# Performance work log

Hardware: AMD Instinct MI355X
Metric: run time of the kernel (lower is better)

## Reference

```python
import jax, jax.numpy as jnp
import numpy as np

B, CIN, H, W = 32, 16, 32, 128
COUT = 128


def _run_direction(x_hwbc, p):
    # x_hwbc: (H, W, B, CIN); scan order is raster (top-to-bottom, left-to-right).
    # Predecessors: dim0 = cell above (previous row), dim1 = cell to the left.
    xi = jnp.einsum('hwbc,oc->hwbo', x_hwbc, p['w_ii'])
    xf = jnp.einsum('hwbc,oc->hwbo', x_hwbc, p['w_if'])
    xg = jnp.einsum('hwbc,oc->hwbo', x_hwbc, p['w_ig'])
    xo = jnp.einsum('hwbc,oc->hwbo', x_hwbc, p['w_io'])
    Wdim, Bdim = x_hwbc.shape[1], x_hwbc.shape[2]
    O = p['w_hi'].shape[0]
    ws0, ws1 = p['ws'][0], p['ws'][1]

    def branch(xi_, xf_, xg_, xo_, c, h):
        i = jax.nn.sigmoid(xi_ + h @ p['w_hi'].T + p['b_i'])
        f = jax.nn.sigmoid(xf_ + h @ p['w_hf'].T + p['b_f'])
        g = jnp.tanh(xg_ + h @ p['w_hg'].T + p['b_g'])
        o = jax.nn.sigmoid(xo_ + h @ p['w_ho'].T + p['b_o'])
        cn = f * c + i * g
        return cn, o * jnp.tanh(cn)

    def col_step(carry, inp):
        c_left, h_left = carry                      # (B, O)
        xi_, xf_, xg_, xo_, c_top, h_top = inp      # each (B, O)
        c0, h0 = branch(xi_, xf_, xg_, xo_, c_top, h_top)   # vertical predecessor
        c1, h1 = branch(xi_, xf_, xg_, xo_, c_left, h_left) # horizontal predecessor
        ct = ws0 * c0 + ws1 * c1 + p['bias']
        ht = ws0 * h0 + ws1 * h1 + p['bias']
        return (ct, ht), (ct, ht)

    def row_step(carry, row):
        c_top, h_top = carry                        # (W, B, O)
        xi_r, xf_r, xg_r, xo_r = row
        z = jnp.zeros((Bdim, O), xi_r.dtype)
        _, (c_row, h_row) = jax.lax.scan(col_step, (z, z), (xi_r, xf_r, xg_r, xo_r, c_top, h_top))
        return (c_row, h_row), h_row

    z_row = jnp.zeros((Wdim, Bdim, O), x_hwbc.dtype)
    _, h_all = jax.lax.scan(row_step, (z_row, z_row), (xi, xf, xg, xo))
    return h_all  # (H, W, B, O)


def _forward(x, w_ii, w_hi, b_i, w_if, w_hf, b_f, w_ig, w_hg, b_g,
             w_io, w_ho, b_o, weighted_sum, bias):
    # Four scan directions realized by flipping the grid (lr_tb, rl_tb, lr_bt, rl_bt).
    x_hwbc = jnp.transpose(x, (2, 3, 0, 1))  # (H, W, B, CIN)
    flips = [(False, False), (False, True), (True, False), (True, True)]
    outs = []
    for d, (fy, fx) in enumerate(flips):
        xd = x_hwbc
        if fy:
            xd = xd[::-1]
        if fx:
            xd = xd[:, ::-1]
        p = {'w_ii': w_ii[d], 'w_hi': w_hi[d], 'b_i': b_i[d],
             'w_if': w_if[d], 'w_hf': w_hf[d], 'b_f': b_f[d],
             'w_ig': w_ig[d], 'w_hg': w_hg[d], 'b_g': b_g[d],
             'w_io': w_io[d], 'w_ho': w_ho[d], 'b_o': b_o[d],
             'ws': weighted_sum[d], 'bias': bias[d]}
        h = _run_direction(xd, p)
        if fy:
            h = h[::-1]
        if fx:
            h = h[:, ::-1]
        outs.append(h)
    h4 = jnp.stack(outs)                      # (4, H, W, B, O)
    return jnp.transpose(h4, (0, 4, 3, 1, 2)) # (4, O, B, H, W)


def setup_inputs() -> dict:
    key = jax.random.key(0)
    ks = jax.random.split(key, 16)
    xw = lambda k: jax.random.normal(k, (4, COUT, CIN), jnp.float32) * 0.05
    hw = lambda k: jax.random.normal(k, (4, COUT, COUT), jnp.float32) * 0.05
    bb = lambda k: jax.random.normal(k, (4, COUT), jnp.float32) * 0.05
    return {
        'x': jax.random.normal(ks[0], (B, CIN, H, W), jnp.float32),
        'w_ii': xw(ks[1]), 'w_hi': hw(ks[2]), 'b_i': bb(ks[3]),
        'w_if': xw(ks[4]), 'w_hf': hw(ks[5]), 'b_f': bb(ks[6]),
        'w_ig': xw(ks[7]), 'w_hg': hw(ks[8]), 'b_g': bb(ks[9]),
        'w_io': xw(ks[10]), 'w_ho': hw(ks[11]), 'b_o': bb(ks[12]),
        'weighted_sum': jax.random.uniform(ks[13], (4, 2), jnp.float32),
        'bias': bb(ks[14]),
    }


def reference(x, w_ii, w_hi, b_i, w_if, w_hf, b_f, w_ig, w_hg, b_g,
              w_io, w_ho, b_o, weighted_sum, bias):
    return _forward(x, w_ii, w_hi, b_i, w_if, w_hf, b_f, w_ig, w_hg, b_g,
                    w_io, w_ho, b_o, weighted_sum, bias)
```

## Files before the change

### kernel.cpp

```cpp
#include <hip/hip_runtime.h>

#define Hh 32
#define Ww 128
#define BB 32
#define CC 16
#define OO 128
#define SPIN_CAP (1 << 23)
#define FSTRIDE 32

typedef __attribute__((ext_vector_type(8))) short short8;
typedef __attribute__((ext_vector_type(4))) float f32x4;

__device__ inline short f2bf(float f) {
    unsigned u = __builtin_bit_cast(unsigned, f);
    unsigned r = (u + 0x7FFFu + ((u >> 16) & 1u)) >> 16;
    return (short)r;
}
__device__ inline float bf2f(short s) {
    unsigned u = ((unsigned)(unsigned short)s) << 16;
    return __builtin_bit_cast(float, u);
}
__device__ inline float rcp_(float x) { return __builtin_amdgcn_rcpf(x); }
__device__ inline float sigm(float x) {
    return rcp_(1.f + __builtin_amdgcn_exp2f(-1.442695041f * x));
}
__device__ inline float tanh_(float x) {
    return 1.f - 2.f * rcp_(__builtin_amdgcn_exp2f(2.885390082f * x) + 1.f);
}

__device__ inline unsigned long long aload64(const unsigned long long* p) {
    return __hip_atomic_load(p, __ATOMIC_RELAXED, __HIP_MEMORY_SCOPE_AGENT);
}
__device__ inline void astore64(unsigned long long* p, unsigned long long v) {
    __hip_atomic_store(p, v, __ATOMIC_RELAXED, __HIP_MEMORY_SCOPE_AGENT);
}
__device__ inline void astore16(short* p, short v) {
    __hip_atomic_store(p, v, __ATOMIC_RELAXED, __HIP_MEMORY_SCOPE_AGENT);
}
__device__ inline int aloadI(const int* p) {
    return __hip_atomic_load(p, __ATOMIC_RELAXED, __HIP_MEMORY_SCOPE_AGENT);
}
__device__ inline void astoreI(int* p, int v) {
    __hip_atomic_store(p, v, __ATOMIC_RELAXED, __HIP_MEMORY_SCOPE_AGENT);
}

__global__ void mdlstm_init(const float* __restrict__ x, short* __restrict__ xT,
                            int* __restrict__ flags) {
    int idx = blockIdx.x * 256 + threadIdx.x;
    if (blockIdx.x < 64) flags[idx] = 0;
    int w = idx & 127;
    int h = (idx >> 7) & 31;
    int c = (idx >> 12) & 15;
    int b = idx >> 16;
    float v = x[idx];
    xT[((h * Ww + w) * BB + b) * CC + c] = f2bf(v);
}

__global__ void __launch_bounds__(512, 1) mdlstm_main(
    const short* __restrict__ xT,
    const float* __restrict__ w_ii, const float* __restrict__ w_hi, const float* __restrict__ b_i,
    const float* __restrict__ w_if, const float* __restrict__ w_hf, const float* __restrict__ b_f,
    const float* __restrict__ w_ig, const float* __restrict__ w_hg, const float* __restrict__ b_g,
    const float* __restrict__ w_io, const float* __restrict__ w_ho, const float* __restrict__ b_o,
    const float* __restrict__ wsum, const float* __restrict__ bias,
    short* __restrict__ hring, float* __restrict__ cring,
    int* __restrict__ prog, int* __restrict__ cons,
    float* __restrict__ out, int depth)
{
    const int chain = blockIdx.x & 7;
    const int r     = blockIdx.x >> 3;
    const int d     = chain >> 1;
    const int s     = chain & 1;
    const int b0    = s * 16;
    const bool fy   = (d >= 2);
    const bool fx   = (d & 1);
    const int hh    = fy ? (Hh - 1 - r) : r;

    const int tid  = threadIdx.x;
    const int wv   = tid >> 6;
    const int lane = tid & 63;
    const int lr   = lane & 15;
    const int lh   = lane >> 4;
    const int on   = wv * 16 + lr;

    __shared__ short stage[OO * 256];

    const float* whp[4] = {w_hi, w_hf, w_hg, w_ho};
    const float* wip[4] = {w_ii, w_if, w_ig, w_io};
    short8 whf[4][4];
    short8 wif_[4];
#pragma unroll
    for (int g = 0; g < 4; ++g) {
#pragma unroll
        for (int kt = 0; kt < 4; ++kt) {
            const float* p = whp[g] + ((d * OO + on) * OO + kt * 32 + lh * 8);
            short8 f;
#pragma unroll
            for (int j = 0; j < 8; ++j) f[j] = f2bf(p[j]);
            whf[g][kt] = f;
        }
        short8 fi = (short8)(short)0;
        if (lh < 2) {
            const float* p = wip[g] + ((d * OO + on) * CC + lh * 8);
#pragma unroll
            for (int j = 0; j < 8; ++j) fi[j] = f2bf(p[j]);
        }
        wif_[g] = fi;
    }

    const float bi  = b_i[d * OO + on];
    const float bf_ = b_f[d * OO + on];
    const float bg_ = b_g[d * OO + on];
    const float bo_ = b_o[d * OO + on];
    const float bb_ = bias[d * OO + on];
    const float ws0 = wsum[d * 2 + 0];
    const float ws1 = wsum[d * 2 + 1];

    int* topf      = prog + ((d * 32 + (r - 1)) * 2 + s) * FSTRIDE;
    int* myprog    = prog + ((d * 32 + r) * 2 + s) * FSTRIDE;
    int* mycons    = cons + ((d * 32 + r) * 2 + s) * FSTRIDE;
    int* consnext  = cons + ((d * 32 + (r + 1)) * 2 + s) * FSTRIDE;

    const int rbh_me  = ((d * 32 + r)     * 2 + s) * depth * (16 * OO);
    const int rbh_top = ((d * 32 + (r-1)) * 2 + s) * depth * (16 * OO);
    const int rbc_me  = ((d * 32 + r)     * 2 + s) * depth * (OO * 16);
    const int rbc_top = ((d * 32 + (r-1)) * 2 + s) * depth * (OO * 16);
    const int smask   = depth - 1;

    short8 hLf[4];
#pragma unroll
    for (int kt = 0; kt < 4; ++kt) hLf[kt] = (short8)(short)0;
    float cL[4] = {0.f, 0.f, 0.f, 0.f};

    short8 hTfB[4];
#pragma unroll
    for (int kt = 0; kt < 4; ++kt) hTfB[kt] = (short8)(short)0;
    float cTB[4] = {0.f, 0.f, 0.f, 0.f};

    int top_seen = 0, cons_seen = 0;
    const f32x4 zacc = {0.f, 0.f, 0.f, 0.f};

    short8 xf_next = (short8)(short)0;
    {
        const int ww0 = fx ? (Ww - 1) : 0;
        if (lh < 2)
            xf_next = *(const short8*)(xT + ((hh * Ww + ww0) * BB + b0 + lr) * CC + lh * 8);
    }

#pragma unroll 2
    for (int wsc = 0; wsc < Ww; ++wsc) {
        const int ww    = fx ? (Ww - 1 - wsc) : wsc;
        const int slot  = wsc & smask;
        const int wslot = ww & 15;
        const bool evenc = ((wsc & 1) == 0);

        const short8 xf = xf_next;

        short8 hTf[4];
        float cT[4];
        if (r > 0) {
            if (evenc) {
                const int need = wsc + 2;
                if (top_seen < need) {
                    int spin = 0;
                    while (top_seen < need && spin < SPIN_CAP) {
                        const int v = aloadI(topf);
                        if (v < need) { __builtin_amdgcn_s_sleep(1); ++spin; } else top_seen = v;
                    }
                }
                const short* hb = hring + rbh_top + slot * (16 * OO) + lr * OO;
#pragma unroll
                for (int kt = 0; kt < 4; ++kt) {
                    union { unsigned long long q[2]; short8 v; } w;
                    w.q[0] = aload64((const unsigned long long*)(hb + kt * 32 + lh * 8));
                    w.q[1] = aload64((const unsigned long long*)(hb + kt * 32 + lh * 8 + 4));
                    hTf[kt] = w.v;
                }
                const short* hb2 = hb + 16 * OO;
#pragma unroll
                for (int kt = 0; kt < 4; ++kt) {
                    union { unsigned long long q[2]; short8 v; } w;
                    w.q[0] = aload64((const unsigned long long*)(hb2 + kt * 32 + lh * 8));
                    w.q[1] = aload64((const unsigned long long*)(hb2 + kt * 32 + lh * 8 + 4));
                    hTfB[kt] = w.v;
                }
                const unsigned long long* cp =
                    (const unsigned long long*)(cring + rbc_top + slot * (OO * 16) + on * 16 + lh * 4);
                union { unsigned long long q; float f[2]; } c01, c23;
                c01.q = aload64(cp);
                c23.q = aload64(cp + 1);
                cT[0] = c01.f[0]; cT[1] = c01.f[1]; cT[2] = c23.f[0]; cT[3] = c23.f[1];
                const unsigned long long* cpB =
                    (const unsigned long long*)(cring + rbc_top + (slot + 1) * (OO * 16) + on * 16 + lh * 4);
                c01.q = aload64(cpB);
                c23.q = aload64(cpB + 1);
                cTB[0] = c01.f[0]; cTB[1] = c01.f[1]; cTB[2] = c23.f[0]; cTB[3] = c23.f[1];
            } else {
#pragma unroll
                for (int kt = 0; kt < 4; ++kt) hTf[kt] = hTfB[kt];
#pragma unroll
                for (int j = 0; j < 4; ++j) cT[j] = cTB[j];
            }
        } else {
#pragma unroll
            for (int kt = 0; kt < 4; ++kt) hTf[kt] = (short8)(short)0;
#pragma unroll
            for (int j = 0; j < 4; ++j) cT[j] = 0.f;
        }

        f32x4 ax[4], accL[4], accT[4];
#pragma unroll
        for (int g = 0; g < 4; ++g)
            ax[g] = __builtin_amdgcn_mfma_f32_16x16x32_bf16(xf, wif_[g], zacc, 0, 0, 0);
#pragma unroll
        for (int g = 0; g < 4; ++g) {
            f32x4 a = ax[g];
#pragma unroll
            for (int kt = 0; kt < 4; ++kt)
                a = __builtin_amdgcn_mfma_f32_16x16x32_bf16(hLf[kt], whf[g][kt], a, 0, 0, 0);
            accL[g] = a;
        }

        if (wsc + 1 < Ww) {
            const int wwN = fx ? (Ww - 2 - wsc) : (wsc + 1);
            if (lh < 2)
                xf_next = *(const short8*)(xT + ((hh * Ww + wwN) * BB + b0 + lr) * CC + lh * 8);
        }

#pragma unroll
        for (int g = 0; g < 4; ++g) {
            f32x4 a = ax[g];
#pragma unroll
            for (int kt = 0; kt < 4; ++kt)
                a = __builtin_amdgcn_mfma_f32_16x16x32_bf16(hTf[kt], whf[g][kt], a, 0, 0, 0);
            accT[g] = a;
        }

        float ctv[4];
        union { short sh[4]; unsigned long long q; } hpack;
#pragma unroll
        for (int j = 0; j < 4; ++j) {
            float iT = sigm(accT[0][j] + bi);
            float fT = sigm(accT[1][j] + bf_);
            float gT = tanh_(accT[2][j] + bg_);
            float oT = sigm(accT[3][j] + bo_);
            float c0 = fT * cT[j] + iT * gT;
            float h0 = oT * tanh_(c0);

            float iL = sigm(accL[0][j] + bi);
            float fL = sigm(accL[1][j] + bf_);
            float gL = tanh_(accL[2][j] + bg_);
            float oL = sigm(accL[3][j] + bo_);
            float c1 = fL * cL[j] + iL * gL;
            float h1 = oL * tanh_(c1);

            float ct = ws0 * c0 + ws1 * c1 + bb_;
            float ht = ws0 * h0 + ws1 * h1 + bb_;
            cL[j] = ct;
            ctv[j] = ct;
            hpack.sh[j] = f2bf(ht);
        }

        if ((wsc & 15) == 0 && wsc != 0) __syncthreads();

        {
            const int g_on = (on >> 3) & 15;
            *(unsigned long long*)&stage[on * 256 + ((wslot ^ g_on) << 4) + lh * 4] = hpack.q;
        }

        if (r < 31 && evenc && wsc >= depth) {
            const int need = wsc - (depth - 2);
            if (cons_seen < need) {
                int spin = 0;
                while (cons_seen < need && spin < SPIN_CAP) {
                    const int v = aloadI(consnext);
                    if (v < need) { __builtin_amdgcn_s_sleep(1); ++spin; } else cons_seen = v;
                }
            }
        }

        if (r < 31) {
            short* hp = hring + rbh_me + slot * (16 * OO) + on;
#pragma unroll
            for (int j = 0; j < 4; ++j)
                astore16(hp + (lh * 4 + j) * OO, hpack.sh[j]);
            union { float f[2]; unsigned long long q; } p01, p23;
            p01.f[0] = ctv[0]; p01.f[1] = ctv[1];
            p23.f[0] = ctv[2]; p23.f[1] = ctv[3];
            unsigned long long* cp =
                (unsigned long long*)(cring + rbc_me + slot * (OO * 16) + on * 16 + lh * 4);
            astore64(cp, p01.q);
            astore64(cp + 1, p23.q);
        }

        __syncthreads();

        if (!evenc && tid == 0) {
            if (r < 31) astoreI(myprog, wsc + 1);
            if (r > 0)  astoreI(mycons, wsc + 1);
        }

        if (r > 0 && !evenc && wsc < Ww - 1) {
            const int v = aloadI(topf);
            if (v > top_seen) top_seen = v;
        }

#pragma unroll
        for (int kt = 0; kt < 4; ++kt) {
            const int col = ((wslot ^ (kt * 4 + lh)) << 4) + lr;
            short8 f;
#pragma unroll
            for (int jj = 0; jj < 8; ++jj)
                f[jj] = stage[(kt * 32 + lh * 8 + jj) * 256 + col];
            hLf[kt] = f;
        }

        if ((wsc & 15) == 15) {
            const int wbase = ww & ~15;
            const int q  = tid & 3;
            const int r0 = tid >> 2;
#pragma unroll
            for (int i = 0; i < 16; ++i) {
                const int row = r0 + (i << 7);
                const int o = row >> 4;
                const int b = row & 15;
                const int go = (o >> 3) & 15;
                f32x4 v;
#pragma unroll
                for (int k = 0; k < 4; ++k)
                    v[k] = bf2f(stage[o * 256 + (((q * 4 + k) ^ go) << 4) + b]);
                float* op = out + ((size_t)((d * OO + o) * BB + b0 + b)) * (Hh * Ww)
                                + hh * Ww + wbase + q * 4;
                __builtin_nontemporal_store(v, (f32x4*)op);
            }
        }
    }
}

extern "C" void kernel_launch(void* const* d_in, const int* in_sizes, int n_in,
                              void* d_out, int out_size, void* d_ws, size_t ws_size,
                              hipStream_t stream) {
    (void)in_sizes; (void)n_in; (void)out_size;

    const float* x     = (const float*)d_in[0];
    const float* w_ii  = (const float*)d_in[1];
    const float* w_hi  = (const float*)d_in[2];
    const float* b_i   = (const float*)d_in[3];
    const float* w_if  = (const float*)d_in[4];
    const float* w_hf  = (const float*)d_in[5];
    const float* b_f   = (const float*)d_in[6];
    const float* w_ig  = (const float*)d_in[7];
    const float* w_hg  = (const float*)d_in[8];
    const float* b_g   = (const float*)d_in[9];
    const float* w_io  = (const float*)d_in[10];
    const float* w_ho  = (const float*)d_in[11];
    const float* b_o   = (const float*)d_in[12];
    const float* wsum  = (const float*)d_in[13];
    const float* bias  = (const float*)d_in[14];
    float* outp        = (float*)d_out;

    char* ws = (char*)d_ws;
    int*   flags  = (int*)ws;
    short* xTp    = (short*)(ws + (64u << 10));
    const size_t off_h = (64u << 10) + (4u << 20);

    int depth = 8;
    const size_t need8 = off_h + ((size_t)8 << 20) + ((size_t)16 << 20) + (1u << 20);
    if (ws_size < need8) depth = 4;

    short* hringp = (short*)(ws + off_h);
    float* cringp = (float*)(ws + off_h + ((size_t)depth << 20));
    int*   progp  = flags;
    int*   consp  = flags + 256 * FSTRIDE;

    hipLaunchKernelGGL(mdlstm_init, dim3(8192), dim3(256), 0, stream, x, xTp, flags);

    mdlstm_main<<<dim3(256), dim3(512), 0, stream>>>(
        xTp,
        w_ii, w_hi, b_i,
        w_if, w_hf, b_f,
        w_ig, w_hg, b_g,
        w_io, w_ho, b_o,
        wsum, bias,
        hringp, cringp, progp, consp,
        outp, depth);
}
```

Baseline: 1.091 ms.

## Batch vertical-branch gates for column pairs and relayout LDS stage for vector reads

The vertical-predecessor gate MFMAs and activations for two columns are now computed together on even steps, because both top rows are already loaded then. This takes the top-branch work off the serial left-to-right dependency on odd steps. The shared staging buffer is changed to a column-major [w][b][o] layout with an XOR swizzle, so hLf fragments load as single short8 vector reads instead of eight scalar LDS reads. In exchange, the per-element writes and output readback become scattered scalar accesses, register pressure rises from the extra per-pair state, and the load imbalance between even and odd steps grows.

```diff
diff --git a/kernel.cpp b/kernel.cpp
--- a/kernel.cpp
+++ b/kernel.cpp
@@ -83,7 +83,7 @@
     const int lh   = lane >> 4;
     const int on   = wv * 16 + lr;
 
-    __shared__ short stage[OO * 256];
+    __shared__ short stage[16 * 16 * 128];
 
     const float* whp[4] = {w_hi, w_hf, w_hg, w_ho};
     const float* wip[4] = {w_ii, w_if, w_ig, w_io};
@@ -132,19 +132,21 @@
     for (int kt = 0; kt < 4; ++kt) hLf[kt] = (short8)(short)0;
     float cL[4] = {0.f, 0.f, 0.f, 0.f};
 
-    short8 hTfB[4];
-#pragma unroll
-    for (int kt = 0; kt < 4; ++kt) hTfB[kt] = (short8)(short)0;
-    float cTB[4] = {0.f, 0.f, 0.f, 0.f};
+    float c0A[4], h0A[4], c0B[4], h0B[4];
+#pragma unroll
+    for (int j = 0; j < 4; ++j) { c0A[j] = h0A[j] = c0B[j] = h0B[j] = 0.f; }
+    f32x4 axB[4];
 
     int top_seen = 0, cons_seen = 0;
     const f32x4 zacc = {0.f, 0.f, 0.f, 0.f};
 
-    short8 xf_next = (short8)(short)0;
-    {
-        const int ww0 = fx ? (Ww - 1) : 0;
-        if (lh < 2)
-            xf_next = *(const short8*)(xT + ((hh * Ww + ww0) * BB + b0 + lr) * CC + lh * 8);
+    short8 xfA = (short8)(short)0, xfB = (short8)(short)0;
+    short8 xfN0 = (short8)(short)0, xfN1 = (short8)(short)0;
+    if (lh < 2) {
+        const int w0 = fx ? (Ww - 1) : 0;
+        const int w1 = fx ? (Ww - 2) : 1;
+        xfA = *(const short8*)(xT + ((hh * Ww + w0) * BB + b0 + lr) * CC + lh * 8);
+        xfB = *(const short8*)(xT + ((hh * Ww + w1) * BB + b0 + lr) * CC + lh * 8);
     }
 
 #pragma unroll 2
@@ -154,12 +156,10 @@
         const int wslot = ww & 15;
         const bool evenc = ((wsc & 1) == 0);
 
-        const short8 xf = xf_next;
-
-        short8 hTf[4];
-        float cT[4];
-        if (r > 0) {
-            if (evenc) {
+        if (evenc) {
+            short8 hTfA[4], hTfB[4];
+            float cTA[4], cTB[4];
+            if (r > 0) {
                 const int need = wsc + 2;
                 if (top_seen < need) {
                     int spin = 0;
@@ -169,14 +169,14 @@
                     }
                 }
                 const short* hb = hring + rbh_top + slot * (16 * OO) + lr * OO;
+                const short* hb2 = hb + 16 * OO;
 #pragma unroll
                 for (int kt = 0; kt < 4; ++kt) {
                     union { unsigned long long q[2]; short8 v; } w;
                     w.q[0] = aload64((const unsigned long long*)(hb + kt * 32 + lh * 8));
                     w.q[1] = aload64((const unsigned long long*)(hb + kt * 32 + lh * 8 + 4));
-                    hTf[kt] = w.v;
-                }
-                const short* hb2 = hb + 16 * OO;
+                    hTfA[kt] = w.v;
+                }
 #pragma unroll
                 for (int kt = 0; kt < 4; ++kt) {
                     union { unsigned long long q[2]; short8 v; } w;
@@ -189,7 +189,7 @@
                 union { unsigned long long q; float f[2]; } c01, c23;
                 c01.q = aload64(cp);
                 c23.q = aload64(cp + 1);
-                cT[0] = c01.f[0]; cT[1] = c01.f[1]; cT[2] = c23.f[0]; cT[3] = c23.f[1];
+                cTA[0] = c01.f[0]; cTA[1] = c01.f[1]; cTA[2] = c23.f[0]; cTA[3] = c23.f[1];
                 const unsigned long long* cpB =
                     (const unsigned long long*)(cring + rbc_top + (slot + 1) * (OO * 16) + on * 16 + lh * 4);
                 c01.q = aload64(cpB);
@@ -197,56 +197,91 @@
                 cTB[0] = c01.f[0]; cTB[1] = c01.f[1]; cTB[2] = c23.f[0]; cTB[3] = c23.f[1];
             } else {
 #pragma unroll
-                for (int kt = 0; kt < 4; ++kt) hTf[kt] = hTfB[kt];
-#pragma unroll
-                for (int j = 0; j < 4; ++j) cT[j] = cTB[j];
-            }
-        } else {
-#pragma unroll
-            for (int kt = 0; kt < 4; ++kt) hTf[kt] = (short8)(short)0;
-#pragma unroll
-            for (int j = 0; j < 4; ++j) cT[j] = 0.f;
-        }
-
-        f32x4 ax[4], accL[4], accT[4];
-#pragma unroll
-        for (int g = 0; g < 4; ++g)
-            ax[g] = __builtin_amdgcn_mfma_f32_16x16x32_bf16(xf, wif_[g], zacc, 0, 0, 0);
-#pragma unroll
-        for (int g = 0; g < 4; ++g) {
-            f32x4 a = ax[g];
-#pragma unroll
-            for (int kt = 0; kt < 4; ++kt)
-                a = __builtin_amdgcn_mfma_f32_16x16x32_bf16(hLf[kt], whf[g][kt], a, 0, 0, 0);
-            accL[g] = a;
-        }
-
-        if (wsc + 1 < Ww) {
-            const int wwN = fx ? (Ww - 2 - wsc) : (wsc + 1);
-            if (lh < 2)
-                xf_next = *(const short8*)(xT + ((hh * Ww + wwN) * BB + b0 + lr) * CC + lh * 8);
-        }
-
-#pragma unroll
-        for (int g = 0; g < 4; ++g) {
-            f32x4 a = ax[g];
-#pragma unroll
-            for (int kt = 0; kt < 4; ++kt)
-                a = __builtin_amdgcn_mfma_f32_16x16x32_bf16(hTf[kt], whf[g][kt], a, 0, 0, 0);
-            accT[g] = a;
+                for (int kt = 0; kt < 4; ++kt) { hTfA[kt] = (short8)(short)0; hTfB[kt] = (short8)(short)0; }
+#pragma unroll
+                for (int j = 0; j < 4; ++j) { cTA[j] = 0.f; cTB[j] = 0.f; }
+            }
+
+            f32x4 axA[4];
+#pragma unroll
+            for (int g = 0; g < 4; ++g) {
+                axA[g] = __builtin_amdgcn_mfma_f32_16x16x32_bf16(xfA, wif_[g], zacc, 0, 0, 0);
+                axB[g] = __builtin_amdgcn_mfma_f32_16x16x32_bf16(xfB, wif_[g], zacc, 0, 0, 0);
+            }
+
+            if (lh < 2 && wsc + 3 < Ww + 1) {
+                if (wsc + 2 < Ww) {
+                    const int wN0 = fx ? (Ww - 3 - wsc) : (wsc + 2);
+                    xfN0 = *(const short8*)(xT + ((hh * Ww + wN0) * BB + b0 + lr) * CC + lh * 8);
+                }
+                if (wsc + 3 < Ww) {
+                    const int wN1 = fx ? (Ww - 4 - wsc) : (wsc + 3);
+                    xfN1 = *(const short8*)(xT + ((hh * Ww + wN1) * BB + b0 + lr) * CC + lh * 8);
+                }
+            }
+
+            {
+                f32x4 aT[4];
+#pragma unroll
+                for (int g = 0; g < 4; ++g) {
+                    f32x4 a = axA[g];
+#pragma unroll
+                    for (int kt = 0; kt < 4; ++kt)
+                        a = __builtin_amdgcn_mfma_f32_16x16x32_bf16(hTfA[kt], whf[g][kt], a, 0, 0, 0);
+                    aT[g] = a;
+                }
+#pragma unroll
+                for (int j = 0; j < 4; ++j) {
+                    float iT = sigm(aT[0][j] + bi);
+                    float fT = sigm(aT[1][j] + bf_);
+                    float gT = tanh_(aT[2][j] + bg_);
+                    float oT = sigm(aT[3][j] + bo_);
+                    float c0 = fT * cTA[j] + iT * gT;
+                    c0A[j] = c0;
+                    h0A[j] = oT * tanh_(c0);
+                }
+            }
+            {
+                f32x4 aT[4];
+#pragma unroll
+                for (int g = 0; g < 4; ++g) {
+                    f32x4 a = axB[g];
+#pragma unroll
+                    for (int kt = 0; kt < 4; ++kt)
+                        a = __builtin_amdgcn_mfma_f32_16x16x32_bf16(hTfB[kt], whf[g][kt], a, 0, 0, 0);
+                    aT[g] = a;
+                }
+#pragma unroll
+                for (int j = 0; j < 4; ++j) {
+                    float iT = sigm(aT[0][j] + bi);
+                    float fT = sigm(aT[1][j] + bf_);
+                    float gT = tanh_(aT[2][j] + bg_);
+                    float oT = sigm(aT[3][j] + bo_);
+                    float c0 = fT * cTB[j] + iT * gT;
+                    c0B[j] = c0;
+                    h0B[j] = oT * tanh_(c0);
+                }
+            }
+        }
+
+        f32x4 accL[4];
+        {
+#pragma unroll
+            for (int g = 0; g < 4; ++g) {
+                f32x4 a = evenc
+                    ? __builtin_amdgcn_mfma_f32_16x16x32_bf16(xfA, wif_[g], zacc, 0, 0, 0)
+                    : axB[g];
+#pragma unroll
+                for (int kt = 0; kt < 4; ++kt)
+                    a = __builtin_amdgcn_mfma_f32_16x16x32_bf16(hLf[kt], whf[g][kt], a, 0, 0, 0);
+                accL[g] = a;
+            }
         }
 
         float ctv[4];
         union { short sh[4]; unsigned long long q; } hpack;
 #pragma unroll
         for (int j = 0; j < 4; ++j) {
-            float iT = sigm(accT[0][j] + bi);
-            float fT = sigm(accT[1][j] + bf_);
-            float gT = tanh_(accT[2][j] + bg_);
-            float oT = sigm(accT[3][j] + bo_);
-            float c0 = fT * cT[j] + iT * gT;
-            float h0 = oT * tanh_(c0);
-
             float iL = sigm(accL[0][j] + bi);
             float fL = sigm(accL[1][j] + bf_);
             float gL = tanh_(accL[2][j] + bg_);
@@ -254,6 +289,8 @@
             float c1 = fL * cL[j] + iL * gL;
             float h1 = oL * tanh_(c1);
 
+            const float c0 = evenc ? c0A[j] : c0B[j];
+            const float h0 = evenc ? h0A[j] : h0B[j];
             float ct = ws0 * c0 + ws1 * c1 + bb_;
             float ht = ws0 * h0 + ws1 * h1 + bb_;
             cL[j] = ct;
@@ -263,9 +300,10 @@
 
         if ((wsc & 15) == 0 && wsc != 0) __syncthreads();
 
-        {
-            const int g_on = (on >> 3) & 15;
-            *(unsigned long long*)&stage[on * 256 + ((wslot ^ g_on) << 4) + lh * 4] = hpack.q;
+#pragma unroll
+        for (int j = 0; j < 4; ++j) {
+            const int b = lh * 4 + j;
+            stage[wslot * 2048 + b * 128 + ((((on >> 3) ^ b) << 3)) + (on & 7)] = hpack.sh[j];
         }
 
         if (r < 31 && evenc && wsc >= depth) {
@@ -307,13 +345,11 @@
 
 #pragma unroll
         for (int kt = 0; kt < 4; ++kt) {
-            const int col = ((wslot ^ (kt * 4 + lh)) << 4) + lr;
-            short8 f;
-#pragma unroll
-            for (int jj = 0; jj < 8; ++jj)
-                f[jj] = stage[(kt * 32 + lh * 8 + jj) * 256 + col];
-            hLf[kt] = f;
-        }
+            const int idx = wslot * 2048 + lr * 128 + ((((kt << 2) + lh) ^ lr) << 3);
+            hLf[kt] = *(const short8*)&stage[idx];
+        }
+
+        if (!evenc) { xfA = xfN0; xfB = xfN1; }
 
         if ((wsc & 15) == 15) {
             const int wbase = ww & ~15;
@@ -324,11 +360,11 @@
                 const int row = r0 + (i << 7);
                 const int o = row >> 4;
                 const int b = row & 15;
-                const int go = (o >> 3) & 15;
                 f32x4 v;
 #pragma unroll
                 for (int k = 0; k < 4; ++k)
-                    v[k] = bf2f(stage[o * 256 + (((q * 4 + k) ^ go) << 4) + b]);
+                    v[k] = bf2f(stage[(q * 4 + k) * 2048 + b * 128
+                                      + (((o >> 3) ^ b) << 3) + (o & 7)]);
                 float* op = out + ((size_t)((d * OO + o) * BB + b0 + b)) * (Hh * Ww)
                                 + hh * Ww + wbase + q * 4;
                 __builtin_nontemporal_store(v, (f32x4*)op);
```

After: 1.027 ms. 5.8% less time.
